# Optimization experiments

Hardware: AMD Instinct MI355X
Metric: run time of the kernel (lower is better)

## Reference

```python
import jax, jax.numpy as jnp
import numpy as np

NUM_SYM = 50000
NUM_HERB = 50000
N_NODES = NUM_SYM + NUM_HERB
DIM = 128
N_EDGES = 3200000
N_LAYERS = 2


def setup_inputs() -> dict:
    key = jax.random.key(0)
    k1, k2, k3, k4, k5 = jax.random.split(key, 5)
    sym_emb = jax.random.normal(k1, (NUM_SYM, DIM), dtype=jnp.float32)
    herb_emb = jax.random.normal(k2, (NUM_HERB, DIM), dtype=jnp.float32)
    adj_rows = jax.random.randint(k3, (N_EDGES,), 0, N_NODES, dtype=jnp.int32)
    adj_cols = jax.random.randint(k4, (N_EDGES,), 0, N_NODES, dtype=jnp.int32)
    # normalized-Laplacian values are positive; uniform stands in for D^-1/2 A D^-1/2 entries
    adj_vals = jax.random.uniform(k5, (N_EDGES,), dtype=jnp.float32)
    return {"sym_emb": sym_emb, "herb_emb": herb_emb,
            "adj_rows": adj_rows, "adj_cols": adj_cols, "adj_vals": adj_vals}


def _spmm(rows, cols, vals, x):
    # sparse [N,N] @ dense [N,D]: gather source rows, scale, scatter-add to dest rows
    msgs = vals[:, None] * x[cols]              # [E, D]
    return jax.ops.segment_sum(msgs, rows, num_segments=N_NODES)


def reference(sym_emb, herb_emb, adj_rows, adj_cols, adj_vals):
    ego = jnp.concatenate([sym_emb, herb_emb], axis=0)   # [N, D]
    acc = ego
    e = ego
    for _ in range(N_LAYERS):
        e = _spmm(adj_rows, adj_cols, adj_vals, e)
        acc = acc + e
    all_emb = acc / jnp.float32(N_LAYERS + 1)            # mean over stacked layers
    return all_emb[:NUM_SYM], all_emb[NUM_SYM:]
```

## Files before the change

kernel.cpp:

```cpp
#include <hip/hip_runtime.h>

#define NUM_SYM 50000
#define NUM_HERB 50000
#define N_NODES (NUM_SYM + NUM_HERB)
#define DIM 128
#define NB ((N_NODES + 127) / 128)
#define CHUNK 4096
#define PAD 16

typedef float floatx4 __attribute__((ext_vector_type(4)));

__device__ __forceinline__ float bf2f(unsigned short u) {
    return __uint_as_float((unsigned)u << 16);
}
__device__ __forceinline__ unsigned short f2bf(float f) {
    unsigned u = __float_as_uint(f);
    unsigned r = (u + 0x7FFFu + ((u >> 16) & 1u)) >> 16;
    return (unsigned short)r;
}

__global__ __launch_bounds__(1024) void scatter_and_convert(
    const int* __restrict__ rows, const int* __restrict__ cols,
    const float* __restrict__ vals, int E, int CAP, int EB,
    const float* __restrict__ sym, const float* __restrict__ herb,
    int* __restrict__ cur, int2* __restrict__ slots, ushort* __restrict__ xbf)
{
    __shared__ int lh[NB];
    __shared__ int labs[NB];
    if ((int)blockIdx.x >= EB) {
        int i = ((int)blockIdx.x - EB) * 1024 + threadIdx.x;
        const int n4 = N_NODES * DIM / 4;
        if (i >= n4) return;
        const int sym4 = NUM_SYM * DIM / 4;
        float4 v = (i < sym4) ? reinterpret_cast<const float4*>(sym)[i]
                              : reinterpret_cast<const float4*>(herb)[i - sym4];
        ushort4 o;
        o.x = f2bf(v.x); o.y = f2bf(v.y); o.z = f2bf(v.z); o.w = f2bf(v.w);
        reinterpret_cast<ushort4*>(xbf)[i] = o;
        return;
    }
    for (int i = threadIdx.x; i < NB; i += 1024) lh[i] = 0;
    __syncthreads();
    int start = blockIdx.x * CHUNK;
    int end   = min(start + CHUNK, E);
    for (int e = start + threadIdx.x; e < end; e += 1024)
        atomicAdd(&lh[rows[e] >> 7], 1);
    __syncthreads();
    for (int i = threadIdx.x; i < NB; i += 1024) {
        int c = lh[i];
        int resv = c ? atomicAdd(&cur[i * PAD], c) : 0;
        labs[i] = i * CAP + resv;
        lh[i] = 0;
    }
    __syncthreads();
    for (int e = start + threadIdx.x; e < end; e += 1024) {
        int r = rows[e];
        int k = r >> 7;
        int pos = labs[k] + atomicAdd(&lh[k], 1);
        slots[pos] = make_int2(((r & 127) << 17) | cols[e],
                               __float_as_int(vals[e]));
    }
}

__global__ __launch_bounds__(1024) void slots_to_csr(
    const int2* __restrict__ slots, const int* __restrict__ cur, int CAP,
    int* __restrict__ csr, int* __restrict__ rowptr, int* __restrict__ rowend)
{
    __shared__ int h[128];
    int b = blockIdx.x, t = threadIdx.x;
    int n = cur[b * PAD];
    size_t sb = (size_t)b * CAP;
    if (t < 128) h[t] = 0;
    __syncthreads();
    for (int j = t; j < n; j += 1024)
        atomicAdd(&h[(unsigned)slots[sb + j].x >> 17], 1);
    __syncthreads();
    int v = (t < 128) ? h[t] : 0;
    for (int o = 1; o < 128; o <<= 1) {
        int x = (t < 128 && t >= o) ? h[t - o] : 0;
        __syncthreads();
        if (t < 128) h[t] += x;
        __syncthreads();
    }
    int cb = b * CAP;
    if (t < 128) {
        int r = b * 128 + t;
        if (r < N_NODES) {
            rowptr[r] = cb + (h[t] - v);
            rowend[r] = cb + h[t];
        }
    }
    __syncthreads();
    if (t < 128) h[t] -= v;
    __syncthreads();
    for (int j = t; j < n; j += 1024) {
        int2 rec = slots[sb + j];
        int bin = (unsigned)rec.x >> 17;
        int pos = cb + atomicAdd(&h[bin], 1);
        unsigned vb = (unsigned)f2bf(__int_as_float(rec.y));
        csr[pos] = (int)((vb << 17) | ((unsigned)rec.x & 0x1FFFFu));
    }
}

__device__ __forceinline__ float unpack_val(int p) {
    return __uint_as_float(((unsigned)p >> 17) << 16);
}

template <bool FUSE_MEAN>
__global__ __launch_bounds__(256) void spmm_csr_bf16(
    const int* __restrict__ csr, const int* __restrict__ rowptr,
    const int* __restrict__ rowend,
    const ushort* __restrict__ xbf,
    const float* __restrict__ sym, const float* __restrict__ herb,
    const ushort* __restrict__ e1bf,
    void* __restrict__ outp)
{
    int wave = blockIdx.x * 4 + (threadIdx.x >> 6);
    int half = (threadIdx.x >> 5) & 1;
    int lane = threadIdx.x & 31;
    int r = wave * 2 + half;
    if (r >= N_NODES) return;

    int j   = rowptr[r];
    int end = rowend[r];

    float4 acc = make_float4(0.f, 0.f, 0.f, 0.f);
    for (; j + 7 < end; j += 8) {
        int p0 = csr[j], p1 = csr[j + 1], p2 = csr[j + 2], p3 = csr[j + 3];
        int p4 = csr[j + 4], p5 = csr[j + 5], p6 = csr[j + 6], p7 = csr[j + 7];
        ushort4 m0 = reinterpret_cast<const ushort4*>(xbf + (size_t)(p0 & 0x1FFFF) * DIM)[lane];
        ushort4 m1 = reinterpret_cast<const ushort4*>(xbf + (size_t)(p1 & 0x1FFFF) * DIM)[lane];
        ushort4 m2 = reinterpret_cast<const ushort4*>(xbf + (size_t)(p2 & 0x1FFFF) * DIM)[lane];
        ushort4 m3 = reinterpret_cast<const ushort4*>(xbf + (size_t)(p3 & 0x1FFFF) * DIM)[lane];
        ushort4 m4 = reinterpret_cast<const ushort4*>(xbf + (size_t)(p4 & 0x1FFFF) * DIM)[lane];
        ushort4 m5 = reinterpret_cast<const ushort4*>(xbf + (size_t)(p5 & 0x1FFFF) * DIM)[lane];
        ushort4 m6 = reinterpret_cast<const ushort4*>(xbf + (size_t)(p6 & 0x1FFFF) * DIM)[lane];
        ushort4 m7 = reinterpret_cast<const ushort4*>(xbf + (size_t)(p7 & 0x1FFFF) * DIM)[lane];
        float v0 = unpack_val(p0), v1 = unpack_val(p1);
        float v2 = unpack_val(p2), v3 = unpack_val(p3);
        float v4 = unpack_val(p4), v5 = unpack_val(p5);
        float v6 = unpack_val(p6), v7 = unpack_val(p7);
        acc.x += v0 * bf2f(m0.x) + v1 * bf2f(m1.x) + v2 * bf2f(m2.x) + v3 * bf2f(m3.x)
               + v4 * bf2f(m4.x) + v5 * bf2f(m5.x) + v6 * bf2f(m6.x) + v7 * bf2f(m7.x);
        acc.y += v0 * bf2f(m0.y) + v1 * bf2f(m1.y) + v2 * bf2f(m2.y) + v3 * bf2f(m3.y)
               + v4 * bf2f(m4.y) + v5 * bf2f(m5.y) + v6 * bf2f(m6.y) + v7 * bf2f(m7.y);
        acc.z += v0 * bf2f(m0.z) + v1 * bf2f(m1.z) + v2 * bf2f(m2.z) + v3 * bf2f(m3.z)
               + v4 * bf2f(m4.z) + v5 * bf2f(m5.z) + v6 * bf2f(m6.z) + v7 * bf2f(m7.z);
        acc.w += v0 * bf2f(m0.w) + v1 * bf2f(m1.w) + v2 * bf2f(m2.w) + v3 * bf2f(m3.w)
               + v4 * bf2f(m4.w) + v5 * bf2f(m5.w) + v6 * bf2f(m6.w) + v7 * bf2f(m7.w);
    }
    for (; j + 3 < end; j += 4) {
        int p0 = csr[j], p1 = csr[j + 1], p2 = csr[j + 2], p3 = csr[j + 3];
        ushort4 m0 = reinterpret_cast<const ushort4*>(xbf + (size_t)(p0 & 0x1FFFF) * DIM)[lane];
        ushort4 m1 = reinterpret_cast<const ushort4*>(xbf + (size_t)(p1 & 0x1FFFF) * DIM)[lane];
        ushort4 m2 = reinterpret_cast<const ushort4*>(xbf + (size_t)(p2 & 0x1FFFF) * DIM)[lane];
        ushort4 m3 = reinterpret_cast<const ushort4*>(xbf + (size_t)(p3 & 0x1FFFF) * DIM)[lane];
        float v0 = unpack_val(p0), v1 = unpack_val(p1);
        float v2 = unpack_val(p2), v3 = unpack_val(p3);
        acc.x += v0 * bf2f(m0.x) + v1 * bf2f(m1.x) + v2 * bf2f(m2.x) + v3 * bf2f(m3.x);
        acc.y += v0 * bf2f(m0.y) + v1 * bf2f(m1.y) + v2 * bf2f(m2.y) + v3 * bf2f(m3.y);
        acc.z += v0 * bf2f(m0.z) + v1 * bf2f(m1.z) + v2 * bf2f(m2.z) + v3 * bf2f(m3.z);
        acc.w += v0 * bf2f(m0.w) + v1 * bf2f(m1.w) + v2 * bf2f(m2.w) + v3 * bf2f(m3.w);
    }
    for (; j < end; ++j) {
        int p0 = csr[j];
        float v0 = unpack_val(p0);
        ushort4 m0 = reinterpret_cast<const ushort4*>(xbf + (size_t)(p0 & 0x1FFFF) * DIM)[lane];
        acc.x += v0 * bf2f(m0.x);
        acc.y += v0 * bf2f(m0.y);
        acc.z += v0 * bf2f(m0.z);
        acc.w += v0 * bf2f(m0.w);
    }

    if (FUSE_MEAN) {
        const float4* egorow = (r < NUM_SYM)
            ? reinterpret_cast<const float4*>(sym  + (size_t)r * DIM)
            : reinterpret_cast<const float4*>(herb + (size_t)(r - NUM_SYM) * DIM);
        float4 g = egorow[lane];
        ushort4 a = reinterpret_cast<const ushort4*>(e1bf + (size_t)r * DIM)[lane];
        const float s = 1.0f / 3.0f;
        floatx4 o;
        o.x = (g.x + bf2f(a.x) + acc.x) * s;
        o.y = (g.y + bf2f(a.y) + acc.y) * s;
        o.z = (g.z + bf2f(a.z) + acc.z) * s;
        o.w = (g.w + bf2f(a.w) + acc.w) * s;
        __builtin_nontemporal_store(o,
            reinterpret_cast<floatx4*>((float*)outp + (size_t)r * DIM) + lane);
    } else {
        ushort4 o;
        o.x = f2bf(acc.x); o.y = f2bf(acc.y); o.z = f2bf(acc.z); o.w = f2bf(acc.w);
        reinterpret_cast<ushort4*>((ushort*)outp + (size_t)r * DIM)[lane] = o;
    }
}

__global__ __launch_bounds__(256) void spmm_scatter(
    const int* __restrict__ rows, const int* __restrict__ cols,
    const float* __restrict__ vals, int n_edges,
    const float* __restrict__ xa, const float* __restrict__ xb,
    float* __restrict__ out)
{
    int gid = blockIdx.x * 256 + threadIdx.x;
    int edge = gid >> 5;
    if (edge >= n_edges) return;
    int sub = gid & 31;
    int c = cols[edge];
    int r = rows[edge];
    float v = vals[edge];
    const float* xrow = (c < NUM_SYM) ? (xa + (size_t)c * DIM)
                                      : (xb + (size_t)(c - NUM_SYM) * DIM);
    float4 m = reinterpret_cast<const float4*>(xrow)[sub];
    float* o = out + (size_t)r * DIM + (size_t)sub * 4;
    unsafeAtomicAdd(o + 0, v * m.x);
    unsafeAtomicAdd(o + 1, v * m.y);
    unsafeAtomicAdd(o + 2, v * m.z);
    unsafeAtomicAdd(o + 3, v * m.w);
}

__global__ __launch_bounds__(256) void finalize_mean(
    const float* __restrict__ sym, const float* __restrict__ herb,
    const float* __restrict__ e1, float* __restrict__ out)
{
    int i = blockIdx.x * 256 + threadIdx.x;
    const int n4 = N_NODES * DIM / 4;
    if (i >= n4) return;
    const int sym4 = NUM_SYM * DIM / 4;
    float4 e = (i < sym4) ? reinterpret_cast<const float4*>(sym)[i]
                          : reinterpret_cast<const float4*>(herb)[i - sym4];
    float4 a = reinterpret_cast<const float4*>(e1)[i];
    float4 b = reinterpret_cast<float4*>(out)[i];
    const float s = 1.0f / 3.0f;
    float4 r;
    r.x = (e.x + a.x + b.x) * s;
    r.y = (e.y + a.y + b.y) * s;
    r.z = (e.z + a.z + b.z) * s;
    r.w = (e.w + a.w + b.w) * s;
    reinterpret_cast<float4*>(out)[i] = r;
}

extern "C" void kernel_launch(void* const* d_in, const int* in_sizes, int n_in,
                              void* d_out, int out_size, void* d_ws, size_t ws_size,
                              hipStream_t stream) {
    const float* sym  = (const float*)d_in[0];
    const float* herb = (const float*)d_in[1];
    const int*   rows = (const int*)d_in[2];
    const int*   cols = (const int*)d_in[3];
    const float* vals = (const float*)d_in[4];
    const int E = in_sizes[2];
    float* out = (float*)d_out;

    int CAP = (int)(((long)E / NB) * 9 / 8);
    CAP = (CAP + 31) / 32 * 32;
    if (CAP < 512) CAP = 512;

    char* ws = (char*)d_ws;
    auto align256 = [](size_t x) { return (x + 255) & ~(size_t)255; };
    const size_t xbf_bytes  = (size_t)N_NODES * DIM * sizeof(ushort);
    const size_t slot_off   = align256(xbf_bytes);
    const size_t slot_bytes = (size_t)NB * CAP * 8 > xbf_bytes
                            ? (size_t)NB * CAP * 8 : xbf_bytes;
    const size_t csr_off    = align256(slot_off + slot_bytes);
    const size_t rowptr_off = align256(csr_off + (size_t)NB * CAP * 4);
    const size_t rowend_off = align256(rowptr_off + (size_t)N_NODES * 4);
    const size_t cur_off    = align256(rowend_off + (size_t)N_NODES * 4);
    const size_t required   = cur_off + (size_t)NB * PAD * 4;

    if (ws_size < required || E >= (1 << 22)) {
        float* e1 = (float*)ws;
        const size_t e1_bytes = (size_t)N_NODES * DIM * sizeof(float);
        hipMemsetAsync(e1, 0, e1_bytes, stream);
        hipMemsetAsync(out, 0, e1_bytes, stream);
        const int spmm_blocks = (E * 32 + 255) / 256;
        spmm_scatter<<<spmm_blocks, 256, 0, stream>>>(rows, cols, vals, E, sym, herb, e1);
        spmm_scatter<<<spmm_blocks, 256, 0, stream>>>(rows, cols, vals, E,
                                                      e1, e1 + (size_t)NUM_SYM * DIM, out);
        const int n4 = N_NODES * DIM / 4;
        finalize_mean<<<(n4 + 255) / 256, 256, 0, stream>>>(sym, herb, e1, out);
        return;
    }

    ushort* xbf    = (ushort*)ws;
    int2*   slots  = (int2*)(ws + slot_off);
    ushort* e1bf   = (ushort*)(ws + slot_off);
    int*    csr    = (int*)(ws + csr_off);
    int*    rowptr = (int*)(ws + rowptr_off);
    int*    rowend = (int*)(ws + rowend_off);
    int*    cur    = (int*)(ws + cur_off);

    hipMemsetAsync(cur, 0, (size_t)NB * PAD * 4, stream);
    const int EB   = (E + CHUNK - 1) / CHUNK;
    const int n4   = N_NODES * DIM / 4;
    const int CONV = (n4 + 1023) / 1024;
    scatter_and_convert<<<EB + CONV, 1024, 0, stream>>>(rows, cols, vals, E, CAP, EB,
                                                        sym, herb, cur, slots, xbf);

    slots_to_csr<<<NB, 1024, 0, stream>>>(slots, cur, CAP, csr, rowptr, rowend);

    const int blocks = (N_NODES / 2 + 3) / 4;
    spmm_csr_bf16<false><<<blocks, 256, 0, stream>>>(csr, rowptr, rowend, xbf,
                                                     nullptr, nullptr, nullptr, e1bf);
    spmm_csr_bf16<true><<<blocks, 256, 0, stream>>>(csr, rowptr, rowend, e1bf,
                                                    sym, herb, e1bf, out);
}
```

Measured before the change: 432.0 us.

## Fuse CSR construction into SpMM blocks via per-bucket LDS sort

Drops the separate slots_to_csr kernel and the global CSR, rowptr and rowend arrays. Each SpMM block now loads its 128-row bucket of keys and bf16 values straight into registers. It counting-sorts them by row into shared memory, then gathers rows with each half-wave handling 4 rows. Edge records are split into a 4-byte key array and a 2-byte bf16 value array to cut scatter traffic. The trade-offs are that the bucket sort is repeated in both layers, blocks are large (1024 threads, 128 rows) with a sort phase before the gather, and buckets larger than the LDS capacity fall back to the slow path.

New measurement: 489.8 us. +13.4%, slower.

```diff
diff --git a/kernel.cpp b/kernel.cpp
--- a/kernel.cpp
+++ b/kernel.cpp
@@ -7,6 +7,7 @@
 #define NB ((N_NODES + 127) / 128)
 #define CHUNK 4096
 #define PAD 16
+#define LDSCAP 6144
 
 typedef float floatx4 __attribute__((ext_vector_type(4)));
 
@@ -23,7 +24,8 @@
     const int* __restrict__ rows, const int* __restrict__ cols,
     const float* __restrict__ vals, int E, int CAP, int EB,
     const float* __restrict__ sym, const float* __restrict__ herb,
-    int* __restrict__ cur, int2* __restrict__ slots, ushort* __restrict__ xbf)
+    int* __restrict__ cur, int* __restrict__ keys, ushort* __restrict__ bvals,
+    ushort* __restrict__ xbf)
 {
     __shared__ int lh[NB];
     __shared__ int labs[NB];
@@ -57,23 +59,41 @@
         int r = rows[e];
         int k = r >> 7;
         int pos = labs[k] + atomicAdd(&lh[k], 1);
-        slots[pos] = make_int2(((r & 127) << 17) | cols[e],
-                               __float_as_int(vals[e]));
-    }
-}
-
-__global__ __launch_bounds__(1024) void slots_to_csr(
-    const int2* __restrict__ slots, const int* __restrict__ cur, int CAP,
-    int* __restrict__ csr, int* __restrict__ rowptr, int* __restrict__ rowend)
-{
+        keys[pos]  = ((r & 127) << 17) | cols[e];
+        bvals[pos] = f2bf(vals[e]);
+    }
+}
+
+template <int MODE>
+__global__ __launch_bounds__(1024, 8) void spmm_bucket(
+    const int* __restrict__ keys, const ushort* __restrict__ bvals,
+    const int* __restrict__ cur, int CAP,
+    const ushort* __restrict__ xbf,
+    const float* __restrict__ sym, const float* __restrict__ herb,
+    const ushort* __restrict__ e1bf,
+    void* __restrict__ outp)
+{
+    __shared__ int csrl[LDSCAP];
     __shared__ int h[128];
+    __shared__ int rs[129];
     int b = blockIdx.x, t = threadIdx.x;
     int n = cur[b * PAD];
+    if (n > CAP) n = CAP;
     size_t sb = (size_t)b * CAP;
+
+    int    k[6];
+    ushort w[6];
+    #pragma unroll
+    for (int q = 0; q < 6; ++q) {
+        int j = t + (q << 10);
+        if (j < n) { k[q] = keys[sb + j]; w[q] = bvals[sb + j]; }
+        else       { k[q] = -1; }
+    }
     if (t < 128) h[t] = 0;
     __syncthreads();
-    for (int j = t; j < n; j += 1024)
-        atomicAdd(&h[(unsigned)slots[sb + j].x >> 17], 1);
+    #pragma unroll
+    for (int q = 0; q < 6; ++q)
+        if (k[q] != -1) atomicAdd(&h[(unsigned)k[q] >> 17], 1);
     __syncthreads();
     int v = (t < 128) ? h[t] : 0;
     for (int o = 1; o < 128; o <<= 1) {
@@ -82,114 +102,85 @@
         if (t < 128) h[t] += x;
         __syncthreads();
     }
-    int cb = b * CAP;
-    if (t < 128) {
-        int r = b * 128 + t;
-        if (r < N_NODES) {
-            rowptr[r] = cb + (h[t] - v);
-            rowend[r] = cb + h[t];
-        }
-    }
+    if (t < 128) rs[t] = h[t] - v;
+    if (t == 0)  rs[128] = n;
     __syncthreads();
     if (t < 128) h[t] -= v;
     __syncthreads();
-    for (int j = t; j < n; j += 1024) {
-        int2 rec = slots[sb + j];
-        int bin = (unsigned)rec.x >> 17;
-        int pos = cb + atomicAdd(&h[bin], 1);
-        unsigned vb = (unsigned)f2bf(__int_as_float(rec.y));
-        csr[pos] = (int)((vb << 17) | ((unsigned)rec.x & 0x1FFFFu));
-    }
-}
-
-__device__ __forceinline__ float unpack_val(int p) {
-    return __uint_as_float(((unsigned)p >> 17) << 16);
-}
-
-template <bool FUSE_MEAN>
-__global__ __launch_bounds__(256) void spmm_csr_bf16(
-    const int* __restrict__ csr, const int* __restrict__ rowptr,
-    const int* __restrict__ rowend,
-    const ushort* __restrict__ xbf,
-    const float* __restrict__ sym, const float* __restrict__ herb,
-    const ushort* __restrict__ e1bf,
-    void* __restrict__ outp)
-{
-    int wave = blockIdx.x * 4 + (threadIdx.x >> 6);
-    int half = (threadIdx.x >> 5) & 1;
-    int lane = threadIdx.x & 31;
-    int r = wave * 2 + half;
-    if (r >= N_NODES) return;
-
-    int j   = rowptr[r];
-    int end = rowend[r];
-
-    float4 acc = make_float4(0.f, 0.f, 0.f, 0.f);
-    for (; j + 7 < end; j += 8) {
-        int p0 = csr[j], p1 = csr[j + 1], p2 = csr[j + 2], p3 = csr[j + 3];
-        int p4 = csr[j + 4], p5 = csr[j + 5], p6 = csr[j + 6], p7 = csr[j + 7];
-        ushort4 m0 = reinterpret_cast<const ushort4*>(xbf + (size_t)(p0 & 0x1FFFF) * DIM)[lane];
-        ushort4 m1 = reinterpret_cast<const ushort4*>(xbf + (size_t)(p1 & 0x1FFFF) * DIM)[lane];
-        ushort4 m2 = reinterpret_cast<const ushort4*>(xbf + (size_t)(p2 & 0x1FFFF) * DIM)[lane];
-        ushort4 m3 = reinterpret_cast<const ushort4*>(xbf + (size_t)(p3 & 0x1FFFF) * DIM)[lane];
-        ushort4 m4 = reinterpret_cast<const ushort4*>(xbf + (size_t)(p4 & 0x1FFFF) * DIM)[lane];
-        ushort4 m5 = reinterpret_cast<const ushort4*>(xbf + (size_t)(p5 & 0x1FFFF) * DIM)[lane];
-        ushort4 m6 = reinterpret_cast<const ushort4*>(xbf + (size_t)(p6 & 0x1FFFF) * DIM)[lane];
-        ushort4 m7 = reinterpret_cast<const ushort4*>(xbf + (size_t)(p7 & 0x1FFFF) * DIM)[lane];
-        float v0 = unpack_val(p0), v1 = unpack_val(p1);
-        float v2 = unpack_val(p2), v3 = unpack_val(p3);
-        float v4 = unpack_val(p4), v5 = unpack_val(p5);
-        float v6 = unpack_val(p6), v7 = unpack_val(p7);
-        acc.x += v0 * bf2f(m0.x) + v1 * bf2f(m1.x) + v2 * bf2f(m2.x) + v3 * bf2f(m3.x)
-               + v4 * bf2f(m4.x) + v5 * bf2f(m5.x) + v6 * bf2f(m6.x) + v7 * bf2f(m7.x);
-        acc.y += v0 * bf2f(m0.y) + v1 * bf2f(m1.y) + v2 * bf2f(m2.y) + v3 * bf2f(m3.y)
-               + v4 * bf2f(m4.y) + v5 * bf2f(m5.y) + v6 * bf2f(m6.y) + v7 * bf2f(m7.y);
-        acc.z += v0 * bf2f(m0.z) + v1 * bf2f(m1.z) + v2 * bf2f(m2.z) + v3 * bf2f(m3.z)
-               + v4 * bf2f(m4.z) + v5 * bf2f(m5.z) + v6 * bf2f(m6.z) + v7 * bf2f(m7.z);
-        acc.w += v0 * bf2f(m0.w) + v1 * bf2f(m1.w) + v2 * bf2f(m2.w) + v3 * bf2f(m3.w)
-               + v4 * bf2f(m4.w) + v5 * bf2f(m5.w) + v6 * bf2f(m6.w) + v7 * bf2f(m7.w);
-    }
-    for (; j + 3 < end; j += 4) {
-        int p0 = csr[j], p1 = csr[j + 1], p2 = csr[j + 2], p3 = csr[j + 3];
-        ushort4 m0 = reinterpret_cast<const ushort4*>(xbf + (size_t)(p0 & 0x1FFFF) * DIM)[lane];
-        ushort4 m1 = reinterpret_cast<const ushort4*>(xbf + (size_t)(p1 & 0x1FFFF) * DIM)[lane];
-        ushort4 m2 = reinterpret_cast<const ushort4*>(xbf + (size_t)(p2 & 0x1FFFF) * DIM)[lane];
-        ushort4 m3 = reinterpret_cast<const ushort4*>(xbf + (size_t)(p3 & 0x1FFFF) * DIM)[lane];
-        float v0 = unpack_val(p0), v1 = unpack_val(p1);
-        float v2 = unpack_val(p2), v3 = unpack_val(p3);
-        acc.x += v0 * bf2f(m0.x) + v1 * bf2f(m1.x) + v2 * bf2f(m2.x) + v3 * bf2f(m3.x);
-        acc.y += v0 * bf2f(m0.y) + v1 * bf2f(m1.y) + v2 * bf2f(m2.y) + v3 * bf2f(m3.y);
-        acc.z += v0 * bf2f(m0.z) + v1 * bf2f(m1.z) + v2 * bf2f(m2.z) + v3 * bf2f(m3.z);
-        acc.w += v0 * bf2f(m0.w) + v1 * bf2f(m1.w) + v2 * bf2f(m2.w) + v3 * bf2f(m3.w);
-    }
-    for (; j < end; ++j) {
-        int p0 = csr[j];
-        float v0 = unpack_val(p0);
-        ushort4 m0 = reinterpret_cast<const ushort4*>(xbf + (size_t)(p0 & 0x1FFFF) * DIM)[lane];
-        acc.x += v0 * bf2f(m0.x);
-        acc.y += v0 * bf2f(m0.y);
-        acc.z += v0 * bf2f(m0.z);
-        acc.w += v0 * bf2f(m0.w);
-    }
-
-    if (FUSE_MEAN) {
-        const float4* egorow = (r < NUM_SYM)
-            ? reinterpret_cast<const float4*>(sym  + (size_t)r * DIM)
-            : reinterpret_cast<const float4*>(herb + (size_t)(r - NUM_SYM) * DIM);
-        float4 g = egorow[lane];
-        ushort4 a = reinterpret_cast<const ushort4*>(e1bf + (size_t)r * DIM)[lane];
-        const float s = 1.0f / 3.0f;
-        floatx4 o;
-        o.x = (g.x + bf2f(a.x) + acc.x) * s;
-        o.y = (g.y + bf2f(a.y) + acc.y) * s;
-        o.z = (g.z + bf2f(a.z) + acc.z) * s;
-        o.w = (g.w + bf2f(a.w) + acc.w) * s;
-        __builtin_nontemporal_store(o,
-            reinterpret_cast<floatx4*>((float*)outp + (size_t)r * DIM) + lane);
-    } else {
-        ushort4 o;
-        o.x = f2bf(acc.x); o.y = f2bf(acc.y); o.z = f2bf(acc.z); o.w = f2bf(acc.w);
-        reinterpret_cast<ushort4*>((ushort*)outp + (size_t)r * DIM)[lane] = o;
+    #pragma unroll
+    for (int q = 0; q < 6; ++q)
+        if (k[q] != -1) {
+            int bin = (unsigned)k[q] >> 17;
+            int pos = atomicAdd(&h[bin], 1);
+            csrl[pos] = (int)(((unsigned)w[q] << 17) | ((unsigned)k[q] & 0x1FFFFu));
+        }
+    __syncthreads();
+
+    int hw = t >> 5, lane = t & 31;
+    for (int q = 0; q < 4; ++q) {
+        int rl = hw * 4 + q;
+        int rowg = b * 128 + rl;
+        if (rowg >= N_NODES) break;
+        int j = rs[rl], endr = rs[rl + 1];
+        float4 acc = make_float4(0.f, 0.f, 0.f, 0.f);
+        for (; j + 7 < endr; j += 8) {
+            int p0 = csrl[j],     p1 = csrl[j + 1], p2 = csrl[j + 2], p3 = csrl[j + 3];
+            int p4 = csrl[j + 4], p5 = csrl[j + 5], p6 = csrl[j + 6], p7 = csrl[j + 7];
+            ushort4 m0 = reinterpret_cast<const ushort4*>(xbf + (size_t)(p0 & 0x1FFFF) * DIM)[lane];
+            ushort4 m1 = reinterpret_cast<const ushort4*>(xbf + (size_t)(p1 & 0x1FFFF) * DIM)[lane];
+            ushort4 m2 = reinterpret_cast<const ushort4*>(xbf + (size_t)(p2 & 0x1FFFF) * DIM)[lane];
+            ushort4 m3 = reinterpret_cast<const ushort4*>(xbf + (size_t)(p3 & 0x1FFFF) * DIM)[lane];
+            ushort4 m4 = reinterpret_cast<const ushort4*>(xbf + (size_t)(p4 & 0x1FFFF) * DIM)[lane];
+            ushort4 m5 = reinterpret_cast<const ushort4*>(xbf + (size_t)(p5 & 0x1FFFF) * DIM)[lane];
+            ushort4 m6 = reinterpret_cast<const ushort4*>(xbf + (size_t)(p6 & 0x1FFFF) * DIM)[lane];
+            ushort4 m7 = reinterpret_cast<const ushort4*>(xbf + (size_t)(p7 & 0x1FFFF) * DIM)[lane];
+            float v0 = bf2f((unsigned short)((unsigned)p0 >> 17 << 1 >> 1));
+            v0 = __uint_as_float(((unsigned)p0 >> 17) << 16);
+            float v1 = __uint_as_float(((unsigned)p1 >> 17) << 16);
+            float v2 = __uint_as_float(((unsigned)p2 >> 17) << 16);
+            float v3 = __uint_as_float(((unsigned)p3 >> 17) << 16);
+            float v4 = __uint_as_float(((unsigned)p4 >> 17) << 16);
+            float v5 = __uint_as_float(((unsigned)p5 >> 17) << 16);
+            float v6 = __uint_as_float(((unsigned)p6 >> 17) << 16);
+            float v7 = __uint_as_float(((unsigned)p7 >> 17) << 16);
+            acc.x += v0 * bf2f(m0.x) + v1 * bf2f(m1.x) + v2 * bf2f(m2.x) + v3 * bf2f(m3.x)
+                   + v4 * bf2f(m4.x) + v5 * bf2f(m5.x) + v6 * bf2f(m6.x) + v7 * bf2f(m7.x);
+            acc.y += v0 * bf2f(m0.y) + v1 * bf2f(m1.y) + v2 * bf2f(m2.y) + v3 * bf2f(m3.y)
+                   + v4 * bf2f(m4.y) + v5 * bf2f(m5.y) + v6 * bf2f(m6.y) + v7 * bf2f(m7.y);
+            acc.z += v0 * bf2f(m0.z) + v1 * bf2f(m1.z) + v2 * bf2f(m2.z) + v3 * bf2f(m3.z)
+                   + v4 * bf2f(m4.z) + v5 * bf2f(m5.z) + v6 * bf2f(m6.z) + v7 * bf2f(m7.z);
+            acc.w += v0 * bf2f(m0.w) + v1 * bf2f(m1.w) + v2 * bf2f(m2.w) + v3 * bf2f(m3.w)
+                   + v4 * bf2f(m4.w) + v5 * bf2f(m5.w) + v6 * bf2f(m6.w) + v7 * bf2f(m7.w);
+        }
+        for (; j < endr; ++j) {
+            int p0 = csrl[j];
+            float v0 = __uint_as_float(((unsigned)p0 >> 17) << 16);
+            ushort4 m0 = reinterpret_cast<const ushort4*>(xbf + (size_t)(p0 & 0x1FFFF) * DIM)[lane];
+            acc.x += v0 * bf2f(m0.x);
+            acc.y += v0 * bf2f(m0.y);
+            acc.z += v0 * bf2f(m0.z);
+            acc.w += v0 * bf2f(m0.w);
+        }
+
+        if (MODE == 0) {
+            ushort4 o;
+            o.x = f2bf(acc.x); o.y = f2bf(acc.y); o.z = f2bf(acc.z); o.w = f2bf(acc.w);
+            reinterpret_cast<ushort4*>((ushort*)outp + (size_t)rowg * DIM)[lane] = o;
+        } else {
+            const float4* egorow = (rowg < NUM_SYM)
+                ? reinterpret_cast<const float4*>(sym  + (size_t)rowg * DIM)
+                : reinterpret_cast<const float4*>(herb + (size_t)(rowg - NUM_SYM) * DIM);
+            float4 g = egorow[lane];
+            ushort4 a = reinterpret_cast<const ushort4*>(e1bf + (size_t)rowg * DIM)[lane];
+            const float s = 1.0f / 3.0f;
+            floatx4 o;
+            o.x = (g.x + bf2f(a.x) + acc.x) * s;
+            o.y = (g.y + bf2f(a.y) + acc.y) * s;
+            o.z = (g.z + bf2f(a.z) + acc.z) * s;
+            o.w = (g.w + bf2f(a.w) + acc.w) * s;
+            __builtin_nontemporal_store(o,
+                reinterpret_cast<floatx4*>((float*)outp + (size_t)rowg * DIM) + lane);
+        }
     }
 }
 
@@ -255,16 +246,13 @@
     char* ws = (char*)d_ws;
     auto align256 = [](size_t x) { return (x + 255) & ~(size_t)255; };
     const size_t xbf_bytes  = (size_t)N_NODES * DIM * sizeof(ushort);
-    const size_t slot_off   = align256(xbf_bytes);
-    const size_t slot_bytes = (size_t)NB * CAP * 8 > xbf_bytes
-                            ? (size_t)NB * CAP * 8 : xbf_bytes;
-    const size_t csr_off    = align256(slot_off + slot_bytes);
-    const size_t rowptr_off = align256(csr_off + (size_t)NB * CAP * 4);
-    const size_t rowend_off = align256(rowptr_off + (size_t)N_NODES * 4);
-    const size_t cur_off    = align256(rowend_off + (size_t)N_NODES * 4);
+    const size_t keys_off   = align256(xbf_bytes);
+    const size_t bvals_off  = align256(keys_off + (size_t)NB * CAP * 4);
+    const size_t e1_off     = align256(bvals_off + (size_t)NB * CAP * 2);
+    const size_t cur_off    = align256(e1_off + xbf_bytes);
     const size_t required   = cur_off + (size_t)NB * PAD * 4;
 
-    if (ws_size < required || E >= (1 << 22)) {
+    if (ws_size < required || E >= (1 << 22) || CAP > LDSCAP) {
         float* e1 = (float*)ws;
         const size_t e1_bytes = (size_t)N_NODES * DIM * sizeof(float);
         hipMemsetAsync(e1, 0, e1_bytes, stream);
@@ -278,26 +266,21 @@
         return;
     }
 
-    ushort* xbf    = (ushort*)ws;
-    int2*   slots  = (int2*)(ws + slot_off);
-    ushort* e1bf   = (ushort*)(ws + slot_off);
-    int*    csr    = (int*)(ws + csr_off);
-    int*    rowptr = (int*)(ws + rowptr_off);
-    int*    rowend = (int*)(ws + rowend_off);
-    int*    cur    = (int*)(ws + cur_off);
+    ushort* xbf   = (ushort*)ws;
+    int*    keys  = (int*)(ws + keys_off);
+    ushort* bvals = (ushort*)(ws + bvals_off);
+    ushort* e1bf  = (ushort*)(ws + e1_off);
+    int*    cur   = (int*)(ws + cur_off);
 
     hipMemsetAsync(cur, 0, (size_t)NB * PAD * 4, stream);
     const int EB   = (E + CHUNK - 1) / CHUNK;
     const int n4   = N_NODES * DIM / 4;
     const int CONV = (n4 + 1023) / 1024;
     scatter_and_convert<<<EB + CONV, 1024, 0, stream>>>(rows, cols, vals, E, CAP, EB,
-                                                        sym, herb, cur, slots, xbf);
-
-    slots_to_csr<<<NB, 1024, 0, stream>>>(slots, cur, CAP, csr, rowptr, rowend);
-
-    const int blocks = (N_NODES / 2 + 3) / 4;
-    spmm_csr_bf16<false><<<blocks, 256, 0, stream>>>(csr, rowptr, rowend, xbf,
-                                                     nullptr, nullptr, nullptr, e1bf);
-    spmm_csr_bf16<true><<<blocks, 256, 0, stream>>>(csr, rowptr, rowend, e1bf,
-                                                    sym, herb, e1bf, out);
-}
+                                                        sym, herb, cur, keys, bvals, xbf);
+
+    spmm_bucket<0><<<NB, 1024, 0, stream>>>(keys, bvals, cur, CAP, xbf,
+                                            nullptr, nullptr, nullptr, e1bf);
+    spmm_bucket<1><<<NB, 1024, 0, stream>>>(keys, bvals, cur, CAP, e1bf,
+                                            sym, herb, e1bf, out);
+}
```
